# Kernel optimization log

Measured on AMD Instinct MI355X. Metric: run time of the kernel, lower is better.

The kernel has to match this reference:

```python
import jax, jax.numpy as jnp
import numpy as np

T, B, I, H, NCLS = 1024, 256, 128, 128, 18

def setup_inputs() -> dict:
    key = jax.random.key(0)
    ks = jax.random.split(key, 8)
    s = 1.0 / np.sqrt(H)  # torch nn.LSTM/Linear init bound
    inp = jax.random.normal(ks[0], (T, B, I), dtype=jnp.float32)
    hidden = jnp.zeros((1, B, H), dtype=jnp.float32)
    cell = jnp.zeros((1, B, H), dtype=jnp.float32)
    W_ih = jax.random.uniform(ks[1], (4 * H, I), jnp.float32, -s, s)
    W_hh = jax.random.uniform(ks[2], (4 * H, H), jnp.float32, -s, s)
    b_ih = jax.random.uniform(ks[3], (4 * H,), jnp.float32, -s, s)
    b_hh = jax.random.uniform(ks[4], (4 * H,), jnp.float32, -s, s)
    fc_W = jax.random.uniform(ks[5], (NCLS, H), jnp.float32, -s, s)
    fc_b = jax.random.uniform(ks[6], (NCLS,), jnp.float32, -s, s)
    return {"input": inp, "hidden": hidden, "cell": cell, "W_ih": W_ih,
            "W_hh": W_hh, "b_ih": b_ih, "b_hh": b_hh, "fc_W": fc_W, "fc_b": fc_b}

def reference(input, hidden, cell, W_ih, W_hh, b_ih, b_hh, fc_W, fc_b):
    # Single-layer unidirectional LSTM (PyTorch gate order i,f,g,o) + Linear head.
    h0, c0 = hidden[0], cell[0]  # [B,H]
    b = b_ih + b_hh

    def step(carry, x_t):
        h, c = carry
        gates = x_t @ W_ih.T + h @ W_hh.T + b  # [B,4H]
        i, f, g, o = jnp.split(gates, 4, axis=-1)
        i = jax.nn.sigmoid(i)
        f = jax.nn.sigmoid(f)
        g = jnp.tanh(g)
        o = jax.nn.sigmoid(o)
        c = f * c + i * g
        h = o * jnp.tanh(c)
        return (h, c), h

    (hT, cT), hs = jax.lax.scan(step, (h0, c0), input)  # hs: [T,B,H]
    out = hs @ fc_W.T + fc_b  # [T,B,18]
    return (out, (hT[None], cT[None]))
```

## Files before the change

kernel.cpp:

```cpp
#include <hip/hip_runtime.h>
#include <cstdint>
#include <cstddef>

#define TSTEPS 1024
#define NB 256
#define NI 128
#define NH 128
#define NC 18
#define CH 32
#define NCHUNK (TSTEPS/CH)
#define XGS 516

typedef _Float16 f16x8 __attribute__((ext_vector_type(8)));
typedef float    f32x4 __attribute__((ext_vector_type(4)));
typedef _Float16 half2_t __attribute__((ext_vector_type(2)));

__device__ __forceinline__ half2_t as_h2(uint32_t v){
  union { uint32_t u; half2_t h; } cv; cv.u = v; return cv.h;
}
__device__ __forceinline__ uint32_t pku(float a, float b){
  union { half2_t h; uint32_t u; } cv; cv.h.x=(_Float16)a; cv.h.y=(_Float16)b; return cv.u;
}
__device__ __forceinline__ float dot2f(half2_t a, half2_t b, float c){
#if __has_builtin(__builtin_amdgcn_fdot2)
  return __builtin_amdgcn_fdot2(a, b, c, false);
#else
  return c + (float)a.x*(float)b.x + (float)a.y*(float)b.y;
#endif
}
__device__ __forceinline__ float fast_rcp(float x){
#if __has_builtin(__builtin_amdgcn_rcpf)
  return __builtin_amdgcn_rcpf(x);
#else
  return 1.f / x;
#endif
}
__device__ __forceinline__ float sigm(float v){
  return fast_rcp(1.f + __expf(-v));
}
__device__ __forceinline__ float tanhx(float v){
  float r = fast_rcp(1.f + __expf(2.f*v));
  return __builtin_fmaf(-2.f, r, 1.f);
}
__device__ __forceinline__ f16x8 ldrow_f16(const float* base){
  float4 f0 = ((const float4*)base)[0];
  float4 f1 = ((const float4*)base)[1];
  f16x8 r;
  r[0]=(_Float16)f0.x; r[1]=(_Float16)f0.y; r[2]=(_Float16)f0.z; r[3]=(_Float16)f0.w;
  r[4]=(_Float16)f1.x; r[5]=(_Float16)f1.y; r[6]=(_Float16)f1.z; r[7]=(_Float16)f1.w;
  return r;
}
__device__ __forceinline__ void barrier_lds(){
  asm volatile("s_waitcnt lgkmcnt(0)" ::: "memory");
  __builtin_amdgcn_s_barrier();
}

__global__ __launch_bounds__(512, 2) void lstm_mfma(
    const float* __restrict__ x,
    const float* __restrict__ h0,
    const float* __restrict__ c0,
    const float* __restrict__ Wih,
    const float* __restrict__ Whh,
    const float* __restrict__ bih,
    const float* __restrict__ bhh,
    const float* __restrict__ fcW,
    const float* __restrict__ fcb,
    float* __restrict__ out,
    float* __restrict__ hT,
    float* __restrict__ cT)
{
  const int b    = blockIdx.x;
  const int tid  = threadIdx.x;
  const int w    = tid >> 6;
  const int l    = tid & 63;
  const int n    = l & 15;
  const int quad = l >> 4;

  __shared__ __align__(16) _Float16 xs[CH][136];
  __shared__ __align__(16) float    xgp[CH][XGS];
  __shared__ __align__(16) _Float16 hist[CH][128];
  __shared__ __align__(16) uint32_t fcw[NC][66];

  f16x8 whh[4][4], wih[4][4];
#pragma unroll
  for (int q = 0; q < 4; ++q){
    const int row = q*128 + w*16 + n;
#pragma unroll
    for (int kt = 0; kt < 4; ++kt){
      whh[q][kt] = ldrow_f16(Whh + (size_t)row*NH + kt*32 + quad*8);
      wih[q][kt] = ldrow_f16(Wih + (size_t)row*NI + kt*32 + quad*8);
    }
  }
  float biasq[4];
#pragma unroll
  for (int q = 0; q < 4; ++q){
    const int g = q*128 + w*16 + n;
    biasq[q] = bih[g] + bhh[g];
  }
  float cst = c0[(size_t)b*NH + w*16 + n];

  if (tid < 128) hist[CH-1][tid] = (_Float16)h0[(size_t)b*NH + tid];
#pragma unroll
  for (int r = 0; r < 3; ++r){
    int idx = tid + 512*r;
    if (idx < NC*64){
      int j = idx >> 6, k = idx & 63;
      float2 f = ((const float2*)(fcW + (size_t)j*NH))[k];
      fcw[j][k] = pku(f.x, f.y);
    }
  }

  const int ttA = tid >> 5;
  const int ttB = ttA + 16;
  const int k4  = tid & 31;
  float4 xpA = ((const float4*)(x + ((size_t)ttA*NB + b)*NI))[k4];
  float4 xpB = ((const float4*)(x + ((size_t)ttB*NB + b)*NI))[k4];
  __syncthreads();

  f16x8 afr[4] = { (f16x8)(_Float16)0, (f16x8)(_Float16)0,
                   (f16x8)(_Float16)0, (f16x8)(_Float16)0 };
  float hlast = 0.f;

#pragma unroll 1
  for (int ck = 0; ck < NCHUNK; ++ck){
    const int t0 = ck*CH;

    {
      union { _Float16 h[4]; uint2 u2; } pa, pb;
      pa.h[0]=(_Float16)xpA.x; pa.h[1]=(_Float16)xpA.y;
      pa.h[2]=(_Float16)xpA.z; pa.h[3]=(_Float16)xpA.w;
      *(uint2*)&xs[ttA][4*k4] = pa.u2;
      pb.h[0]=(_Float16)xpB.x; pb.h[1]=(_Float16)xpB.y;
      pb.h[2]=(_Float16)xpB.z; pb.h[3]=(_Float16)xpB.w;
      *(uint2*)&xs[ttB][4*k4] = pb.u2;
    }
    barrier_lds();

    {
      f16x8 xa[2][4];
#pragma unroll
      for (int mt = 0; mt < 2; ++mt)
#pragma unroll
        for (int kt = 0; kt < 4; ++kt)
          xa[mt][kt] = *(const f16x8*)&xs[mt*16 + n][kt*32 + quad*8];

#pragma unroll
      for (int q = 0; q < 4; ++q){
#pragma unroll
        for (int mt = 0; mt < 2; ++mt){
          f32x4 acc = { biasq[q], biasq[q], biasq[q], biasq[q] };
#pragma unroll
          for (int kt = 0; kt < 4; ++kt)
            acc = __builtin_amdgcn_mfma_f32_16x16x32_f16(xa[mt][kt], wih[q][kt], acc, 0, 0, 0);
#pragma unroll
          for (int r = 0; r < 4; ++r)
            xgp[mt*16 + quad*4 + r][(w*16 + n)*4 + q] = acc[r];
        }
      }
    }

    if (ck + 1 < NCHUNK){
      const size_t t1 = (size_t)(t0 + CH);
      xpA = ((const float4*)(x + ((t1 + ttA)*NB + b)*NI))[k4];
      xpB = ((const float4*)(x + ((t1 + ttB)*NB + b)*NI))[k4];
    }
    barrier_lds();

#pragma unroll 4
    for (int tt = 0; tt < CH; ++tt){
      f32x4 sgv = *(const f32x4*)&xgp[tt][(w*16 + n)*4];
      const int rp = (tt + CH - 1) & (CH - 1);
      if (n == 0){
#pragma unroll
        for (int kt = 0; kt < 4; ++kt)
          afr[kt] = *(const f16x8*)&hist[rp][kt*32 + quad*8];
      }
      float gate[4];
#pragma unroll
      for (int q = 0; q < 4; ++q){
        f32x4 aA; aA[0] = sgv[q];
        aA = __builtin_amdgcn_mfma_f32_16x16x32_f16(afr[0], whh[q][0], aA, 0, 0, 0);
        aA = __builtin_amdgcn_mfma_f32_16x16x32_f16(afr[1], whh[q][1], aA, 0, 0, 0);
        f32x4 aB; aB[0] = 0.f;
        aB = __builtin_amdgcn_mfma_f32_16x16x32_f16(afr[2], whh[q][2], aB, 0, 0, 0);
        aB = __builtin_amdgcn_mfma_f32_16x16x32_f16(afr[3], whh[q][3], aB, 0, 0, 0);
        gate[q] = aA[0] + aB[0];
      }
      if (l < 16){
        float iv = sigm(gate[0]);
        float fv = sigm(gate[1]);
        float gv = tanhx(gate[2]);
        float ov = sigm(gate[3]);
        cst = __builtin_fmaf(fv, cst, iv*gv);
        float hv = ov * tanhx(cst);
        hlast = hv;
        hist[tt][w*16 + l] = (_Float16)hv;
      }
      barrier_lds();
      (void)rp;
    }

    {
      const int tt = tid >> 4;
      const int jb = tid & 15;
      const uint4* hb = (const uint4*)&hist[tt][0];
#pragma unroll
      for (int jj = 0; jj < 2; ++jj){
        const int j = jj*16 + jb;
        if (j < NC){
          const uint2* fw = (const uint2*)&fcw[j][0];
          float a0=0.f, a1=0.f, a2=0.f, a3=0.f;
#pragma unroll
          for (int q = 0; q < 4; ++q){
            uint4 v0 = hb[q], v1 = hb[4+q], v2 = hb[8+q], v3 = hb[12+q];
            uint2 f0a = fw[2*q],    f0b = fw[2*q+1];
            uint2 f1a = fw[8+2*q],  f1b = fw[8+2*q+1];
            uint2 f2a = fw[16+2*q], f2b = fw[16+2*q+1];
            uint2 f3a = fw[24+2*q], f3b = fw[24+2*q+1];
            a0 = dot2f(as_h2(f0a.x), as_h2(v0.x), a0);
            a1 = dot2f(as_h2(f1a.x), as_h2(v1.x), a1);
            a2 = dot2f(as_h2(f2a.x), as_h2(v2.x), a2);
            a3 = dot2f(as_h2(f3a.x), as_h2(v3.x), a3);
            a0 = dot2f(as_h2(f0a.y), as_h2(v0.y), a0);
            a1 = dot2f(as_h2(f1a.y), as_h2(v1.y), a1);
            a2 = dot2f(as_h2(f2a.y), as_h2(v2.y), a2);
            a3 = dot2f(as_h2(f3a.y), as_h2(v3.y), a3);
            a0 = dot2f(as_h2(f0b.x), as_h2(v0.z), a0);
            a1 = dot2f(as_h2(f1b.x), as_h2(v1.z), a1);
            a2 = dot2f(as_h2(f2b.x), as_h2(v2.z), a2);
            a3 = dot2f(as_h2(f3b.x), as_h2(v3.z), a3);
            a0 = dot2f(as_h2(f0b.y), as_h2(v0.w), a0);
            a1 = dot2f(as_h2(f1b.y), as_h2(v1.w), a1);
            a2 = dot2f(as_h2(f2b.y), as_h2(v2.w), a2);
            a3 = dot2f(as_h2(f3b.y), as_h2(v3.w), a3);
          }
          out[(size_t)(t0+tt)*NB*NC + (size_t)b*NC + j] =
              (a0+a1) + (a2+a3) + fcb[j];
        }
      }
    }
  }

  if (l < 16){
    hT[(size_t)b*NH + w*16 + l] = hlast;
    cT[(size_t)b*NH + w*16 + l] = cst;
  }
}

extern "C" void kernel_launch(void* const* d_in, const int* in_sizes, int n_in,
                              void* d_out, int out_size, void* d_ws, size_t ws_size,
                              hipStream_t stream) {
  (void)in_sizes; (void)n_in; (void)d_ws; (void)ws_size; (void)out_size;
  const float* x   = (const float*)d_in[0];
  const float* h0  = (const float*)d_in[1];
  const float* c0  = (const float*)d_in[2];
  const float* Wih = (const float*)d_in[3];
  const float* Whh = (const float*)d_in[4];
  const float* bih = (const float*)d_in[5];
  const float* bhh = (const float*)d_in[6];
  const float* fcW = (const float*)d_in[7];
  const float* fcb = (const float*)d_in[8];
  float* out = (float*)d_out;
  float* hT  = out + (size_t)TSTEPS*NB*NC;
  float* cT  = hT + (size_t)NB*NH;
  hipLaunchKernelGGL(lstm_mfma, dim3(NB), dim3(512), 0, stream,
                     x, h0, c0, Wih, Whh, bih, bhh, fcW, fcb, out, hT, cT);
}
```

Before: 822.2 us.

## Interleave next-chunk input projection and FC head into the recurrent step loop

Double-buffers the x-gate buffer and the h history. The next chunk's input projection and the previous chunk's FC head are split into slices that run during idle slots of the serial per-timestep recurrence, instead of as separate phases between chunks. The goal is to hide non-recurrent work behind the latency-bound MFMA/barrier chain and remove the per-chunk serial phases. All lanes now load the h fragments every step, in place of only n==0. This adds LDS traffic and register pressure per step, and may lengthen the critical path of each timestep.

```diff
diff --git a/kernel.cpp b/kernel.cpp
--- a/kernel.cpp
+++ b/kernel.cpp
@@ -54,6 +54,57 @@
   asm volatile("s_waitcnt lgkmcnt(0)" ::: "memory");
   __builtin_amdgcn_s_barrier();
 }
+
+#define X_SLICE(Q) do {                                                          \
+    const int mt_ = s_ & 1;                                                      \
+    f16x8 xa0 = *(const f16x8*)&xs[mt_*16+n][0*32+quad*8];                       \
+    f16x8 xa1 = *(const f16x8*)&xs[mt_*16+n][1*32+quad*8];                       \
+    f16x8 xa2 = *(const f16x8*)&xs[mt_*16+n][2*32+quad*8];                       \
+    f16x8 xa3 = *(const f16x8*)&xs[mt_*16+n][3*32+quad*8];                       \
+    f32x4 acc_ = { biasq[Q], biasq[Q], biasq[Q], biasq[Q] };                     \
+    acc_ = __builtin_amdgcn_mfma_f32_16x16x32_f16(xa0, wih[Q][0], acc_, 0,0,0);  \
+    acc_ = __builtin_amdgcn_mfma_f32_16x16x32_f16(xa1, wih[Q][1], acc_, 0,0,0);  \
+    acc_ = __builtin_amdgcn_mfma_f32_16x16x32_f16(xa2, wih[Q][2], acc_, 0,0,0);  \
+    acc_ = __builtin_amdgcn_mfma_f32_16x16x32_f16(xa3, wih[Q][3], acc_, 0,0,0);  \
+    xgn[mt_*16+quad*4+0][cellw4+(Q)] = acc_[0];                                  \
+    xgn[mt_*16+quad*4+1][cellw4+(Q)] = acc_[1];                                  \
+    xgn[mt_*16+quad*4+2][cellw4+(Q)] = acc_[2];                                  \
+    xgn[mt_*16+quad*4+3][cellw4+(Q)] = acc_[3];                                  \
+  } while(0)
+
+#define HEAD_SLICE(J, ACC, FJ) do {                                              \
+    if ((J)==0 || jb+16 < NC){                                                   \
+      const int j_ = jb + 16*(J);                                                \
+      const uint4* hb_ = (const uint4*)&hist[((ckh-1)*CH + hr) & 63][0];         \
+      const uint2* fw_ = (const uint2*)&fcw[j_][0];                              \
+      uint4 v0=hb_[qh], v1=hb_[4+qh], v2=hb_[8+qh], v3=hb_[12+qh];               \
+      uint2 f0a=fw_[2*qh],    f0b=fw_[2*qh+1];                                   \
+      uint2 f1a=fw_[8+2*qh],  f1b=fw_[8+2*qh+1];                                 \
+      uint2 f2a=fw_[16+2*qh], f2b=fw_[16+2*qh+1];                                \
+      uint2 f3a=fw_[24+2*qh], f3b=fw_[24+2*qh+1];                                \
+      ACC[0]=dot2f(as_h2(f0a.x),as_h2(v0.x),ACC[0]);                             \
+      ACC[1]=dot2f(as_h2(f1a.x),as_h2(v1.x),ACC[1]);                             \
+      ACC[2]=dot2f(as_h2(f2a.x),as_h2(v2.x),ACC[2]);                             \
+      ACC[3]=dot2f(as_h2(f3a.x),as_h2(v3.x),ACC[3]);                             \
+      ACC[0]=dot2f(as_h2(f0a.y),as_h2(v0.y),ACC[0]);                             \
+      ACC[1]=dot2f(as_h2(f1a.y),as_h2(v1.y),ACC[1]);                             \
+      ACC[2]=dot2f(as_h2(f2a.y),as_h2(v2.y),ACC[2]);                             \
+      ACC[3]=dot2f(as_h2(f3a.y),as_h2(v3.y),ACC[3]);                             \
+      ACC[0]=dot2f(as_h2(f0b.x),as_h2(v0.z),ACC[0]);                             \
+      ACC[1]=dot2f(as_h2(f1b.x),as_h2(v1.z),ACC[1]);                             \
+      ACC[2]=dot2f(as_h2(f2b.x),as_h2(v2.z),ACC[2]);                             \
+      ACC[3]=dot2f(as_h2(f3b.x),as_h2(v3.z),ACC[3]);                             \
+      ACC[0]=dot2f(as_h2(f0b.y),as_h2(v0.w),ACC[0]);                             \
+      ACC[1]=dot2f(as_h2(f1b.y),as_h2(v1.w),ACC[1]);                             \
+      ACC[2]=dot2f(as_h2(f2b.y),as_h2(v2.w),ACC[2]);                             \
+      ACC[3]=dot2f(as_h2(f3b.y),as_h2(v3.w),ACC[3]);                             \
+      if (qh == 3){                                                              \
+        out[(size_t)((ckh-1)*CH + hr)*NB*NC + (size_t)b*NC + j_] =               \
+            (ACC[0]+ACC[1]) + (ACC[2]+ACC[3]) + (FJ);                            \
+        ACC[0]=0.f; ACC[1]=0.f; ACC[2]=0.f; ACC[3]=0.f;                          \
+      }                                                                          \
+    }                                                                            \
+  } while(0)
 
 __global__ __launch_bounds__(512, 2) void lstm_mfma(
     const float* __restrict__ x,
@@ -75,12 +126,12 @@
   const int l    = tid & 63;
   const int n    = l & 15;
   const int quad = l >> 4;
+  const int cellw4 = (w*16 + n)*4;
 
   __shared__ __align__(16) _Float16 xs[CH][136];
-  __shared__ __align__(16) float    xgp[CH][XGS];
-  __shared__ __align__(16) _Float16 hist[CH][128];
+  __shared__ __align__(16) float    xgp[2][CH][XGS];
+  __shared__ __align__(16) _Float16 hist[64][128];
   __shared__ __align__(16) uint32_t fcw[NC][66];
-
   f16x8 whh[4][4], wih[4][4];
 #pragma unroll
   for (int q = 0; q < 4; ++q){
@@ -99,7 +150,7 @@
   }
   float cst = c0[(size_t)b*NH + w*16 + n];
 
-  if (tid < 128) hist[CH-1][tid] = (_Float16)h0[(size_t)b*NH + tid];
+  if (tid < 128) hist[63][tid] = (_Float16)h0[(size_t)b*NH + tid];
 #pragma unroll
   for (int r = 0; r < 3; ++r){
     int idx = tid + 512*r;
@@ -110,6 +161,12 @@
     }
   }
 
+  const int jb = tid & 15;
+  const int hr = tid >> 4;
+  const float fj0 = fcb[jb];
+  const float fj1 = (jb + 16 < NC) ? fcb[jb+16] : 0.f;
+  f32x4 accH0 = {0.f,0.f,0.f,0.f}, accH1 = {0.f,0.f,0.f,0.f};
+
   const int ttA = tid >> 5;
   const int ttB = ttA + 16;
   const int k4  = tid & 31;
@@ -117,15 +174,47 @@
   float4 xpB = ((const float4*)(x + ((size_t)ttB*NB + b)*NI))[k4];
   __syncthreads();
 
-  f16x8 afr[4] = { (f16x8)(_Float16)0, (f16x8)(_Float16)0,
-                   (f16x8)(_Float16)0, (f16x8)(_Float16)0 };
+  {
+    union { _Float16 h[4]; uint2 u2; } pa, pb;
+    pa.h[0]=(_Float16)xpA.x; pa.h[1]=(_Float16)xpA.y;
+    pa.h[2]=(_Float16)xpA.z; pa.h[3]=(_Float16)xpA.w;
+    *(uint2*)&xs[ttA][4*k4] = pa.u2;
+    pb.h[0]=(_Float16)xpB.x; pb.h[1]=(_Float16)xpB.y;
+    pb.h[2]=(_Float16)xpB.z; pb.h[3]=(_Float16)xpB.w;
+    *(uint2*)&xs[ttB][4*k4] = pb.u2;
+  }
+  barrier_lds();
+
+  {
+    f16x8 xa[2][4];
+#pragma unroll
+    for (int mt = 0; mt < 2; ++mt)
+#pragma unroll
+      for (int kt = 0; kt < 4; ++kt)
+        xa[mt][kt] = *(const f16x8*)&xs[mt*16 + n][kt*32 + quad*8];
+#pragma unroll
+    for (int q = 0; q < 4; ++q){
+#pragma unroll
+      for (int mt = 0; mt < 2; ++mt){
+        f32x4 acc = { biasq[q], biasq[q], biasq[q], biasq[q] };
+#pragma unroll
+        for (int kt = 0; kt < 4; ++kt)
+          acc = __builtin_amdgcn_mfma_f32_16x16x32_f16(xa[mt][kt], wih[q][kt], acc, 0, 0, 0);
+#pragma unroll
+        for (int r = 0; r < 4; ++r)
+          xgp[0][mt*16 + quad*4 + r][cellw4 + q] = acc[r];
+      }
+    }
+  }
+  xpA = ((const float4*)(x + ((size_t)(CH+ttA)*NB + b)*NI))[k4];
+  xpB = ((const float4*)(x + ((size_t)(CH+ttB)*NB + b)*NI))[k4];
+  barrier_lds();
+
   float hlast = 0.f;
 
 #pragma unroll 1
   for (int ck = 0; ck < NCHUNK; ++ck){
-    const int t0 = ck*CH;
-
-    {
+    if (ck + 1 < NCHUNK){
       union { _Float16 h[4]; uint2 u2; } pa, pb;
       pa.h[0]=(_Float16)xpA.x; pa.h[1]=(_Float16)xpA.y;
       pa.h[2]=(_Float16)xpA.z; pa.h[3]=(_Float16)xpA.w;
@@ -135,57 +224,53 @@
       *(uint2*)&xs[ttB][4*k4] = pb.u2;
     }
     barrier_lds();
-
-    {
-      f16x8 xa[2][4];
-#pragma unroll
-      for (int mt = 0; mt < 2; ++mt)
-#pragma unroll
-        for (int kt = 0; kt < 4; ++kt)
-          xa[mt][kt] = *(const f16x8*)&xs[mt*16 + n][kt*32 + quad*8];
-
-#pragma unroll
-      for (int q = 0; q < 4; ++q){
-#pragma unroll
-        for (int mt = 0; mt < 2; ++mt){
-          f32x4 acc = { biasq[q], biasq[q], biasq[q], biasq[q] };
-#pragma unroll
-          for (int kt = 0; kt < 4; ++kt)
-            acc = __builtin_amdgcn_mfma_f32_16x16x32_f16(xa[mt][kt], wih[q][kt], acc, 0, 0, 0);
-#pragma unroll
-          for (int r = 0; r < 4; ++r)
-            xgp[mt*16 + quad*4 + r][(w*16 + n)*4 + q] = acc[r];
-        }
-      }
-    }
-
-    if (ck + 1 < NCHUNK){
-      const size_t t1 = (size_t)(t0 + CH);
-      xpA = ((const float4*)(x + ((t1 + ttA)*NB + b)*NI))[k4];
-      xpB = ((const float4*)(x + ((t1 + ttB)*NB + b)*NI))[k4];
-    }
-    barrier_lds();
+    if (ck + 2 < NCHUNK){
+      const size_t t2 = (size_t)(ck + 2)*CH;
+      xpA = ((const float4*)(x + ((t2 + ttA)*NB + b)*NI))[k4];
+      xpB = ((const float4*)(x + ((t2 + ttB)*NB + b)*NI))[k4];
+    }
+
+    float (*xgc)[XGS] = xgp[ck & 1];
+    float (*xgn)[XGS] = xgp[(ck + 1) & 1];
+    const int tbase = ck*CH;
+    const int ckh = ck;
 
 #pragma unroll 4
     for (int tt = 0; tt < CH; ++tt){
-      f32x4 sgv = *(const f32x4*)&xgp[tt][(w*16 + n)*4];
-      const int rp = (tt + CH - 1) & (CH - 1);
-      if (n == 0){
-#pragma unroll
-        for (int kt = 0; kt < 4; ++kt)
-          afr[kt] = *(const f16x8*)&hist[rp][kt*32 + quad*8];
-      }
+      f32x4 sgv = *(const f32x4*)&xgc[tt][cellw4];
+      const _Float16* hprev = &hist[(tbase + tt + 63) & 63][0];
+      f16x8 afr0 = *(const f16x8*)&hprev[0*32 + quad*8];
+      f16x8 afr1 = *(const f16x8*)&hprev[1*32 + quad*8];
+      f16x8 afr2 = *(const f16x8*)&hprev[2*32 + quad*8];
+      f16x8 afr3 = *(const f16x8*)&hprev[3*32 + quad*8];
       float gate[4];
 #pragma unroll
       for (int q = 0; q < 4; ++q){
         f32x4 aA; aA[0] = sgv[q];
-        aA = __builtin_amdgcn_mfma_f32_16x16x32_f16(afr[0], whh[q][0], aA, 0, 0, 0);
-        aA = __builtin_amdgcn_mfma_f32_16x16x32_f16(afr[1], whh[q][1], aA, 0, 0, 0);
+        aA = __builtin_amdgcn_mfma_f32_16x16x32_f16(afr0, whh[q][0], aA, 0, 0, 0);
+        aA = __builtin_amdgcn_mfma_f32_16x16x32_f16(afr1, whh[q][1], aA, 0, 0, 0);
         f32x4 aB; aB[0] = 0.f;
-        aB = __builtin_amdgcn_mfma_f32_16x16x32_f16(afr[2], whh[q][2], aB, 0, 0, 0);
-        aB = __builtin_amdgcn_mfma_f32_16x16x32_f16(afr[3], whh[q][3], aB, 0, 0, 0);
+        aB = __builtin_amdgcn_mfma_f32_16x16x32_f16(afr2, whh[q][2], aB, 0, 0, 0);
+        aB = __builtin_amdgcn_mfma_f32_16x16x32_f16(afr3, whh[q][3], aB, 0, 0, 0);
         gate[q] = aA[0] + aB[0];
       }
+
+      if ((tt & 3) == 0 && ck + 1 < NCHUNK){
+        const int s_ = tt >> 2;
+        switch (s_ >> 1){
+          case 0: X_SLICE(0); break;
+          case 1: X_SLICE(1); break;
+          case 2: X_SLICE(2); break;
+          case 3: X_SLICE(3); break;
+        }
+      }
+      if ((tt & 3) == 2 && ck >= 1){
+        const int s_ = (tt - 2) >> 2;
+        const int qh = s_ & 3;
+        if (s_ < 4) HEAD_SLICE(0, accH0, fj0);
+        else        HEAD_SLICE(1, accH1, fj1);
+      }
+
       if (l < 16){
         float iv = sigm(gate[0]);
         float fv = sigm(gate[1]);
@@ -194,50 +279,19 @@
         cst = __builtin_fmaf(fv, cst, iv*gv);
         float hv = ov * tanhx(cst);
         hlast = hv;
-        hist[tt][w*16 + l] = (_Float16)hv;
+        hist[(tbase + tt) & 63][w*16 + l] = (_Float16)hv;
       }
       barrier_lds();
-      (void)rp;
-    }
-
-    {
-      const int tt = tid >> 4;
-      const int jb = tid & 15;
-      const uint4* hb = (const uint4*)&hist[tt][0];
-#pragma unroll
-      for (int jj = 0; jj < 2; ++jj){
-        const int j = jj*16 + jb;
-        if (j < NC){
-          const uint2* fw = (const uint2*)&fcw[j][0];
-          float a0=0.f, a1=0.f, a2=0.f, a3=0.f;
-#pragma unroll
-          for (int q = 0; q < 4; ++q){
-            uint4 v0 = hb[q], v1 = hb[4+q], v2 = hb[8+q], v3 = hb[12+q];
-            uint2 f0a = fw[2*q],    f0b = fw[2*q+1];
-            uint2 f1a = fw[8+2*q],  f1b = fw[8+2*q+1];
-            uint2 f2a = fw[16+2*q], f2b = fw[16+2*q+1];
-            uint2 f3a = fw[24+2*q], f3b = fw[24+2*q+1];
-            a0 = dot2f(as_h2(f0a.x), as_h2(v0.x), a0);
-            a1 = dot2f(as_h2(f1a.x), as_h2(v1.x), a1);
-            a2 = dot2f(as_h2(f2a.x), as_h2(v2.x), a2);
-            a3 = dot2f(as_h2(f3a.x), as_h2(v3.x), a3);
-            a0 = dot2f(as_h2(f0a.y), as_h2(v0.y), a0);
-            a1 = dot2f(as_h2(f1a.y), as_h2(v1.y), a1);
-            a2 = dot2f(as_h2(f2a.y), as_h2(v2.y), a2);
-            a3 = dot2f(as_h2(f3a.y), as_h2(v3.y), a3);
-            a0 = dot2f(as_h2(f0b.x), as_h2(v0.z), a0);
-            a1 = dot2f(as_h2(f1b.x), as_h2(v1.z), a1);
-            a2 = dot2f(as_h2(f2b.x), as_h2(v2.z), a2);
-            a3 = dot2f(as_h2(f3b.x), as_h2(v3.z), a3);
-            a0 = dot2f(as_h2(f0b.y), as_h2(v0.w), a0);
-            a1 = dot2f(as_h2(f1b.y), as_h2(v1.w), a1);
-            a2 = dot2f(as_h2(f2b.y), as_h2(v2.w), a2);
-            a3 = dot2f(as_h2(f3b.y), as_h2(v3.w), a3);
-          }
-          out[(size_t)(t0+tt)*NB*NC + (size_t)b*NC + j] =
-              (a0+a1) + (a2+a3) + fcb[j];
-        }
-      }
+    }
+  }
+
+  {
+    const int ckh = NCHUNK;
+#pragma unroll
+    for (int s_ = 0; s_ < 8; ++s_){
+      const int qh = s_ & 3;
+      if (s_ < 4) HEAD_SLICE(0, accH0, fj0);
+      else        HEAD_SLICE(1, accH1, fj1);
     }
   }
 
```

Result: slower. 852.5 us (+3.7%).

## Warp-specialize LSTM: recurrent waves overlap input GEMM and FC head

Applied to the files above, without the earlier changes.

Splits the block's 8 waves into 4 recurrent waves and 4 helper waves. Each recurrent wave now owns 32 hidden cells using W_hh fragments. The helper waves hold W_ih fragments and, inside the per-timestep barrier loop, stage the next chunk of x, compute its input projection into a double-buffered xgp, and run the FC head for the previous chunk. This removes the serial per-chunk input GEMM and head phases from the critical path. It also folds log2e scaling into the weights so the activations can use exp2, and XOR-swizzles the 64-row hidden history. The cost is that each recurrent wave does twice the MFMA work per step, and the helper work must fit inside the recurrent step time.

```diff
diff --git a/kernel.cpp b/kernel.cpp
--- a/kernel.cpp
+++ b/kernel.cpp
@@ -11,6 +11,9 @@
 #define NCHUNK (TSTEPS/CH)
 #define XGS 516
 
+#define LOG2E_F    1.44269504088896f
+#define TWO_LOG2E_F 2.88539008177793f
+
 typedef _Float16 f16x8 __attribute__((ext_vector_type(8)));
 typedef float    f32x4 __attribute__((ext_vector_type(4)));
 typedef _Float16 half2_t __attribute__((ext_vector_type(2)));
@@ -35,25 +38,72 @@
   return 1.f / x;
 #endif
 }
-__device__ __forceinline__ float sigm(float v){
-  return fast_rcp(1.f + __expf(-v));
-}
-__device__ __forceinline__ float tanhx(float v){
-  float r = fast_rcp(1.f + __expf(2.f*v));
-  return __builtin_fmaf(-2.f, r, 1.f);
-}
-__device__ __forceinline__ f16x8 ldrow_f16(const float* base){
+__device__ __forceinline__ float exp2x(float v){
+#if __has_builtin(__builtin_amdgcn_exp2f)
+  return __builtin_amdgcn_exp2f(v);
+#else
+  return __expf(v * 0.6931471805599453f);
+#endif
+}
+__device__ __forceinline__ float sigm2(float vp){
+  return fast_rcp(1.f + exp2x(-vp));
+}
+__device__ __forceinline__ float tanh2p(float vp){
+  return __builtin_fmaf(-2.f, fast_rcp(1.f + exp2x(vp)), 1.f);
+}
+__device__ __forceinline__ f16x8 ldrow_f16s(const float* base, float s){
   float4 f0 = ((const float4*)base)[0];
   float4 f1 = ((const float4*)base)[1];
   f16x8 r;
-  r[0]=(_Float16)f0.x; r[1]=(_Float16)f0.y; r[2]=(_Float16)f0.z; r[3]=(_Float16)f0.w;
-  r[4]=(_Float16)f1.x; r[5]=(_Float16)f1.y; r[6]=(_Float16)f1.z; r[7]=(_Float16)f1.w;
+  r[0]=(_Float16)(f0.x*s); r[1]=(_Float16)(f0.y*s); r[2]=(_Float16)(f0.z*s); r[3]=(_Float16)(f0.w*s);
+  r[4]=(_Float16)(f1.x*s); r[5]=(_Float16)(f1.y*s); r[6]=(_Float16)(f1.z*s); r[7]=(_Float16)(f1.w*s);
   return r;
 }
 __device__ __forceinline__ void barrier_lds(){
   asm volatile("s_waitcnt lgkmcnt(0)" ::: "memory");
   __builtin_amdgcn_s_barrier();
 }
+
+#define H_GEMM_TILE(CT, MT_, XGN) do {                                             \
+    const _Float16* xr_ = &xs[(MT_)*16 + n][0];                                    \
+    f16x8 xa0_ = *(const f16x8*)&xr_[ 0 + quad*8];                                 \
+    f16x8 xa1_ = *(const f16x8*)&xr_[32 + quad*8];                                 \
+    f16x8 xa2_ = *(const f16x8*)&xr_[64 + quad*8];                                 \
+    f16x8 xa3_ = *(const f16x8*)&xr_[96 + quad*8];                                 \
+    f32x4 acc_ = { biash[CT], biash[CT], biash[CT], biash[CT] };                   \
+    acc_ = __builtin_amdgcn_mfma_f32_16x16x32_f16(xa0_, wfr[CT][0], acc_, 0,0,0);  \
+    acc_ = __builtin_amdgcn_mfma_f32_16x16x32_f16(xa1_, wfr[CT][1], acc_, 0,0,0);  \
+    acc_ = __builtin_amdgcn_mfma_f32_16x16x32_f16(xa2_, wfr[CT][2], acc_, 0,0,0);  \
+    acc_ = __builtin_amdgcn_mfma_f32_16x16x32_f16(xa3_, wfr[CT][3], acc_, 0,0,0);  \
+    float* xw_ = &(XGN)[(MT_)*16 + quad*4][((CT)*16 + n)*4 + hq];                  \
+    xw_[0] = acc_[0]; xw_[XGS] = acc_[1]; xw_[2*XGS] = acc_[2]; xw_[3*XGS] = acc_[3]; \
+  } while(0)
+
+#define STAGE_W(M_, XPV) do {                                                      \
+    union { _Float16 h_[4]; uint2 u_; } pk_;                                       \
+    pk_.h_[0]=(_Float16)(XPV).x; pk_.h_[1]=(_Float16)(XPV).y;                      \
+    pk_.h_[2]=(_Float16)(XPV).z; pk_.h_[3]=(_Float16)(XPV).w;                      \
+    *(uint2*)&xs[hrW][4*(k8 + 8*(M_))] = pk_.u_;                                   \
+  } while(0)
+
+#define HEAD_DOT(JV, CKH, FB) do {                                                 \
+    const int row_ = (((CKH)*CH + hrW) & 63);                                      \
+    const uint4* hb_ = (const uint4*)&hist[row_][0];                               \
+    const int hx4_ = row_ & 7;                                                     \
+    const uint2* fw_ = (const uint2*)&fcw[(JV)][0];                                \
+    float a0_=0.f, a1_=0.f, a2_=0.f, a3_=0.f;                                      \
+    _Pragma("unroll")                                                              \
+    for (int k_ = 0; k_ < 16; ++k_){                                               \
+      uint4 v_ = hb_[k_ ^ hx4_];                                                   \
+      uint2 fa_ = fw_[2*k_], fb2_ = fw_[2*k_+1];                                   \
+      a0_ = dot2f(as_h2(fa_.x),  as_h2(v_.x), a0_);                                \
+      a1_ = dot2f(as_h2(fa_.y),  as_h2(v_.y), a1_);                                \
+      a2_ = dot2f(as_h2(fb2_.x), as_h2(v_.z), a2_);                                \
+      a3_ = dot2f(as_h2(fb2_.y), as_h2(v_.w), a3_);                                \
+    }                                                                              \
+    out[(size_t)((CKH)*CH + hrW)*NB*NC + (size_t)b*NC + (JV)] =                    \
+        (a0_+a1_) + (a2_+a3_) + (FB);                                              \
+  } while(0)
 
 __global__ __launch_bounds__(512, 2) void lstm_mfma(
     const float* __restrict__ x,
@@ -75,31 +125,52 @@
   const int l    = tid & 63;
   const int n    = l & 15;
   const int quad = l >> 4;
+  const bool isR = (w < 4);
+  const bool hi  = (l >= 32);
 
   __shared__ __align__(16) _Float16 xs[CH][136];
-  __shared__ __align__(16) float    xgp[CH][XGS];
-  __shared__ __align__(16) _Float16 hist[CH][128];
+  __shared__ __align__(16) float    xgp[2][CH][XGS];
+  __shared__ __align__(16) _Float16 hist[64][128];
   __shared__ __align__(16) uint32_t fcw[NC][66];
 
-  f16x8 whh[4][4], wih[4][4];
-#pragma unroll
-  for (int q = 0; q < 4; ++q){
-    const int row = q*128 + w*16 + n;
-#pragma unroll
-    for (int kt = 0; kt < 4; ++kt){
-      whh[q][kt] = ldrow_f16(Whh + (size_t)row*NH + kt*32 + quad*8);
-      wih[q][kt] = ldrow_f16(Wih + (size_t)row*NI + kt*32 + quad*8);
+  const int hq   = w - 4;
+  const int tid2 = hq*64 + l;
+  const int hrW  = tid2 >> 3;
+  const int k8   = tid2 & 7;
+  const int jb   = k8;
+
+  float4 xp0, xp1, xp2, xp3;
+  if (!isR){
+    const float* xb = x + ((size_t)hrW*NB + b)*NI;
+    xp0 = ((const float4*)xb)[k8];
+    xp1 = ((const float4*)xb)[k8+8];
+    xp2 = ((const float4*)xb)[k8+16];
+    xp3 = ((const float4*)xb)[k8+24];
+  }
+
+  f16x8 wfr[8][4];
+  float biash[8];
+  {
+    const float* wsrc = isR ? Whh : Wih;
+#pragma unroll
+    for (int f = 0; f < 8; ++f){
+      const int g  = isR ? ((f>>1)*128 + w*32 + (f&1)*16 + n)
+                         : (hq*128 + f*16 + n);
+      const int qq = isR ? (f>>1) : hq;
+      const float sc = (qq == 2) ? TWO_LOG2E_F : LOG2E_F;
+#pragma unroll
+      for (int kt = 0; kt < 4; ++kt)
+        wfr[f][kt] = ldrow_f16s(wsrc + (size_t)g*128 + kt*32 + quad*8, sc);
+      biash[f] = (bih[g] + bhh[g]) * sc;
     }
   }
-  float biasq[4];
-#pragma unroll
-  for (int q = 0; q < 4; ++q){
-    const int g = q*128 + w*16 + n;
-    biasq[q] = bih[g] + bhh[g];
-  }
-  float cst = c0[(size_t)b*NH + w*16 + n];
-
-  if (tid < 128) hist[CH-1][tid] = (_Float16)h0[(size_t)b*NH + tid];
+
+  const int mycell = (isR ? w*32 : 0) + (hi ? 16 : 0) + n;
+  float cst = 0.f;
+  if (isR) cst = c0[(size_t)b*NH + mycell];
+  float hlast = 0.f;
+
+  if (tid < 128) hist[63][tid ^ 56] = (_Float16)h0[(size_t)b*NH + tid];
 #pragma unroll
   for (int r = 0; r < 3; ++r){
     int idx = tid + 512*r;
@@ -109,141 +180,132 @@
       fcw[j][k] = pku(f.x, f.y);
     }
   }
-
-  const int ttA = tid >> 5;
-  const int ttB = ttA + 16;
-  const int k4  = tid & 31;
-  float4 xpA = ((const float4*)(x + ((size_t)ttA*NB + b)*NI))[k4];
-  float4 xpB = ((const float4*)(x + ((size_t)ttB*NB + b)*NI))[k4];
-  __syncthreads();
-
-  f16x8 afr[4] = { (f16x8)(_Float16)0, (f16x8)(_Float16)0,
-                   (f16x8)(_Float16)0, (f16x8)(_Float16)0 };
-  float hlast = 0.f;
+  float fj0 = 0.f, fj1 = 0.f, fj2 = 0.f;
+  if (!isR){ fj0 = fcb[jb]; fj1 = fcb[jb+8]; if (jb < 2) fj2 = fcb[16+jb]; }
+
+  if (!isR){ STAGE_W(0, xp0); STAGE_W(1, xp1); STAGE_W(2, xp2); STAGE_W(3, xp3); }
+  barrier_lds();
+
+  if (!isR){
+    float (*xgn)[XGS] = xgp[0];
+#pragma unroll
+    for (int ct = 0; ct < 8; ++ct)
+#pragma unroll
+      for (int mt = 0; mt < 2; ++mt)
+        H_GEMM_TILE(ct, mt, xgn);
+    const float* xb = x + ((size_t)(CH + hrW)*NB + b)*NI;
+    xp0 = ((const float4*)xb)[k8];
+    xp1 = ((const float4*)xb)[k8+8];
+    xp2 = ((const float4*)xb)[k8+16];
+    xp3 = ((const float4*)xb)[k8+24];
+  }
+  barrier_lds();
 
 #pragma unroll 1
   for (int ck = 0; ck < NCHUNK; ++ck){
-    const int t0 = ck*CH;
-
-    {
-      union { _Float16 h[4]; uint2 u2; } pa, pb;
-      pa.h[0]=(_Float16)xpA.x; pa.h[1]=(_Float16)xpA.y;
-      pa.h[2]=(_Float16)xpA.z; pa.h[3]=(_Float16)xpA.w;
-      *(uint2*)&xs[ttA][4*k4] = pa.u2;
-      pb.h[0]=(_Float16)xpB.x; pb.h[1]=(_Float16)xpB.y;
-      pb.h[2]=(_Float16)xpB.z; pb.h[3]=(_Float16)xpB.w;
-      *(uint2*)&xs[ttB][4*k4] = pb.u2;
-    }
-    barrier_lds();
-
-    {
-      f16x8 xa[2][4];
-#pragma unroll
-      for (int mt = 0; mt < 2; ++mt)
-#pragma unroll
-        for (int kt = 0; kt < 4; ++kt)
-          xa[mt][kt] = *(const f16x8*)&xs[mt*16 + n][kt*32 + quad*8];
-
-#pragma unroll
-      for (int q = 0; q < 4; ++q){
-#pragma unroll
-        for (int mt = 0; mt < 2; ++mt){
-          f32x4 acc = { biasq[q], biasq[q], biasq[q], biasq[q] };
-#pragma unroll
-          for (int kt = 0; kt < 4; ++kt)
-            acc = __builtin_amdgcn_mfma_f32_16x16x32_f16(xa[mt][kt], wih[q][kt], acc, 0, 0, 0);
-#pragma unroll
-          for (int r = 0; r < 4; ++r)
-            xgp[mt*16 + quad*4 + r][(w*16 + n)*4 + q] = acc[r];
+    float (*xgc)[XGS] = xgp[ck & 1];
+    float (*xgn)[XGS] = xgp[(ck + 1) & 1];
+    const int tbase = (ck*CH) & 63;
+
+#pragma unroll 4
+    for (int tt = 0; tt < CH; ++tt){
+      if (isR){
+        const int rrow = (tbase + tt + 63) & 63;
+        const int hx = (rrow & 7) << 3;
+        const _Float16* hp = &hist[rrow][0];
+        f16x8 a0 = *(const f16x8*)&hp[( 0 + quad*8) ^ hx];
+        f16x8 a1 = *(const f16x8*)&hp[(32 + quad*8) ^ hx];
+        f16x8 a2 = *(const f16x8*)&hp[(64 + quad*8) ^ hx];
+        f16x8 a3 = *(const f16x8*)&hp[(96 + quad*8) ^ hx];
+        const int cb4 = (w*32 + n)*4;
+        f32x4 sgA = *(const f32x4*)&xgc[tt][cb4];
+        f32x4 sgB = *(const f32x4*)&xgc[tt][cb4 + 64];
+        float gA[4], gB[4];
+        __builtin_amdgcn_s_setprio(1);
+#pragma unroll
+        for (int q = 0; q < 4; ++q){
+          f32x4 aA; aA[0] = sgA[q];
+          aA = __builtin_amdgcn_mfma_f32_16x16x32_f16(a0, wfr[q*2+0][0], aA, 0,0,0);
+          aA = __builtin_amdgcn_mfma_f32_16x16x32_f16(a1, wfr[q*2+0][1], aA, 0,0,0);
+          f32x4 aB; aB[0] = 0.f;
+          aB = __builtin_amdgcn_mfma_f32_16x16x32_f16(a2, wfr[q*2+0][2], aB, 0,0,0);
+          aB = __builtin_amdgcn_mfma_f32_16x16x32_f16(a3, wfr[q*2+0][3], aB, 0,0,0);
+          gA[q] = aA[0] + aB[0];
+        }
+#pragma unroll
+        for (int q = 0; q < 4; ++q){
+          f32x4 aA; aA[0] = sgB[q];
+          aA = __builtin_amdgcn_mfma_f32_16x16x32_f16(a0, wfr[q*2+1][0], aA, 0,0,0);
+          aA = __builtin_amdgcn_mfma_f32_16x16x32_f16(a1, wfr[q*2+1][1], aA, 0,0,0);
+          f32x4 aB; aB[0] = 0.f;
+          aB = __builtin_amdgcn_mfma_f32_16x16x32_f16(a2, wfr[q*2+1][2], aB, 0,0,0);
+          aB = __builtin_amdgcn_mfma_f32_16x16x32_f16(a3, wfr[q*2+1][3], aB, 0,0,0);
+          gB[q] = aA[0] + aB[0];
+        }
+        __builtin_amdgcn_s_setprio(0);
+        float gi = hi ? gB[0] : gA[0];
+        float gf = hi ? gB[1] : gA[1];
+        float gg = hi ? gB[2] : gA[2];
+        float go = hi ? gB[3] : gA[3];
+        float iv = sigm2(gi);
+        float fv = sigm2(gf);
+        float gv = tanh2p(gg);
+        float ov = sigm2(go);
+        cst = __builtin_fmaf(fv, cst, iv*gv);
+        float hv = ov * tanh2p(cst * TWO_LOG2E_F);
+        hlast = hv;
+        const int wrow = (tbase + tt) & 63;
+        if ((l & 31) < 16)
+          hist[wrow][mycell ^ ((wrow & 7) << 3)] = (_Float16)hv;
+      } else {
+        if (tt == 0){
+          if (ck <= NCHUNK-2){ STAGE_W(0, xp0); STAGE_W(1, xp1); }
+        } else if (tt == 1){
+          if (ck <= NCHUNK-2){ STAGE_W(2, xp2); STAGE_W(3, xp3); }
+        } else if (tt == 3){
+          if (ck <= NCHUNK-3){
+            const float* xb = x + ((size_t)((ck+2)*CH + hrW)*NB + b)*NI;
+            xp0 = ((const float4*)xb)[k8];
+            xp1 = ((const float4*)xb)[k8+8];
+            xp2 = ((const float4*)xb)[k8+16];
+            xp3 = ((const float4*)xb)[k8+24];
+          }
+        } else if (tt >= 4 && tt < 20){
+          if (ck <= NCHUNK-2){
+            const int slice_ = tt - 4;
+            const int mt_ = slice_ & 1;
+            switch (slice_ >> 1){
+              case 0: H_GEMM_TILE(0, mt_, xgn); break;
+              case 1: H_GEMM_TILE(1, mt_, xgn); break;
+              case 2: H_GEMM_TILE(2, mt_, xgn); break;
+              case 3: H_GEMM_TILE(3, mt_, xgn); break;
+              case 4: H_GEMM_TILE(4, mt_, xgn); break;
+              case 5: H_GEMM_TILE(5, mt_, xgn); break;
+              case 6: H_GEMM_TILE(6, mt_, xgn); break;
+              case 7: H_GEMM_TILE(7, mt_, xgn); break;
+            }
+          }
+        } else if (tt == 20){
+          if (ck >= 1) HEAD_DOT(jb, ck-1, fj0);
+        } else if (tt == 21){
+          if (ck >= 1) HEAD_DOT(jb+8, ck-1, fj1);
+        } else if (tt == 22){
+          if (ck >= 1 && jb < 2) HEAD_DOT(16+jb, ck-1, fj2);
         }
       }
+      barrier_lds();
     }
-
-    if (ck + 1 < NCHUNK){
-      const size_t t1 = (size_t)(t0 + CH);
-      xpA = ((const float4*)(x + ((t1 + ttA)*NB + b)*NI))[k4];
-      xpB = ((const float4*)(x + ((t1 + ttB)*NB + b)*NI))[k4];
+  }
+
+  if (isR){
+    if ((l & 31) < 16){
+      hT[(size_t)b*NH + mycell] = hlast;
+      cT[(size_t)b*NH + mycell] = cst;
     }
-    barrier_lds();
-
-#pragma unroll 4
-    for (int tt = 0; tt < CH; ++tt){
-      f32x4 sgv = *(const f32x4*)&xgp[tt][(w*16 + n)*4];
-      const int rp = (tt + CH - 1) & (CH - 1);
-      if (n == 0){
-#pragma unroll
-        for (int kt = 0; kt < 4; ++kt)
-          afr[kt] = *(const f16x8*)&hist[rp][kt*32 + quad*8];
-      }
-      float gate[4];
-#pragma unroll
-      for (int q = 0; q < 4; ++q){
-        f32x4 aA; aA[0] = sgv[q];
-        aA = __builtin_amdgcn_mfma_f32_16x16x32_f16(afr[0], whh[q][0], aA, 0, 0, 0);
-        aA = __builtin_amdgcn_mfma_f32_16x16x32_f16(afr[1], whh[q][1], aA, 0, 0, 0);
-        f32x4 aB; aB[0] = 0.f;
-        aB = __builtin_amdgcn_mfma_f32_16x16x32_f16(afr[2], whh[q][2], aB, 0, 0, 0);
-        aB = __builtin_amdgcn_mfma_f32_16x16x32_f16(afr[3], whh[q][3], aB, 0, 0, 0);
-        gate[q] = aA[0] + aB[0];
-      }
-      if (l < 16){
-        float iv = sigm(gate[0]);
-        float fv = sigm(gate[1]);
-        float gv = tanhx(gate[2]);
-        float ov = sigm(gate[3]);
-        cst = __builtin_fmaf(fv, cst, iv*gv);
-        float hv = ov * tanhx(cst);
-        hlast = hv;
-        hist[tt][w*16 + l] = (_Float16)hv;
-      }
-      barrier_lds();
-      (void)rp;
-    }
-
-    {
-      const int tt = tid >> 4;
-      const int jb = tid & 15;
-      const uint4* hb = (const uint4*)&hist[tt][0];
-#pragma unroll
-      for (int jj = 0; jj < 2; ++jj){
-        const int j = jj*16 + jb;
-        if (j < NC){
-          const uint2* fw = (const uint2*)&fcw[j][0];
-          float a0=0.f, a1=0.f, a2=0.f, a3=0.f;
-#pragma unroll
-          for (int q = 0; q < 4; ++q){
-            uint4 v0 = hb[q], v1 = hb[4+q], v2 = hb[8+q], v3 = hb[12+q];
-            uint2 f0a = fw[2*q],    f0b = fw[2*q+1];
-            uint2 f1a = fw[8+2*q],  f1b = fw[8+2*q+1];
-            uint2 f2a = fw[16+2*q], f2b = fw[16+2*q+1];
-            uint2 f3a = fw[24+2*q], f3b = fw[24+2*q+1];
-            a0 = dot2f(as_h2(f0a.x), as_h2(v0.x), a0);
-            a1 = dot2f(as_h2(f1a.x), as_h2(v1.x), a1);
-            a2 = dot2f(as_h2(f2a.x), as_h2(v2.x), a2);
-            a3 = dot2f(as_h2(f3a.x), as_h2(v3.x), a3);
-            a0 = dot2f(as_h2(f0a.y), as_h2(v0.y), a0);
-            a1 = dot2f(as_h2(f1a.y), as_h2(v1.y), a1);
-            a2 = dot2f(as_h2(f2a.y), as_h2(v2.y), a2);
-            a3 = dot2f(as_h2(f3a.y), as_h2(v3.y), a3);
-            a0 = dot2f(as_h2(f0b.x), as_h2(v0.z), a0);
-            a1 = dot2f(as_h2(f1b.x), as_h2(v1.z), a1);
-            a2 = dot2f(as_h2(f2b.x), as_h2(v2.z), a2);
-            a3 = dot2f(as_h2(f3b.x), as_h2(v3.z), a3);
-            a0 = dot2f(as_h2(f0b.y), as_h2(v0.w), a0);
-            a1 = dot2f(as_h2(f1b.y), as_h2(v1.w), a1);
-            a2 = dot2f(as_h2(f2b.y), as_h2(v2.w), a2);
-            a3 = dot2f(as_h2(f3b.y), as_h2(v3.w), a3);
-          }
-          out[(size_t)(t0+tt)*NB*NC + (size_t)b*NC + j] =
-              (a0+a1) + (a2+a3) + fcb[j];
-        }
-      }
-    }
-  }
-
-  if (l < 16){
-    hT[(size_t)b*NH + w*16 + l] = hlast;
-    cT[(size_t)b*NH + w*16 + l] = cst;
+  } else {
+    HEAD_DOT(jb, NCHUNK-1, fj0);
+    HEAD_DOT(jb+8, NCHUNK-1, fj1);
+    if (jb < 2) HEAD_DOT(16+jb, NCHUNK-1, fj2);
   }
 }
 
```

Measured after the change: 879.0 us. 1.07x slower.

## Interleave gate rows so all lanes compute activations via DPP quad broadcast

Applied to the files above, without the earlier changes.

Gate rows are remapped so each group of four adjacent lanes holds the i, f, g and o pre-activations for one hidden cell. That spreads the nonlinearity work across all 64 lanes instead of 16 lanes doing four activations serially. The log2(e) scale factors are folded into the weights and bias, so each activation needs only a single exp2 and reciprocal with a lane-dependent sign and affine fixup. Gate values are then exchanged with DPP quad broadcasts. The per-step h fragment load is now done by every lane unconditionally, and fp16 rounding of the pre-scaled weights slightly changes precision.

```diff
diff --git a/kernel.cpp b/kernel.cpp
--- a/kernel.cpp
+++ b/kernel.cpp
@@ -11,6 +11,9 @@
 #define NCHUNK (TSTEPS/CH)
 #define XGS 516
 
+#define LOG2E_F     1.44269504088896f
+#define TWO_LOG2E_F 2.88539008177793f
+
 typedef _Float16 f16x8 __attribute__((ext_vector_type(8)));
 typedef float    f32x4 __attribute__((ext_vector_type(4)));
 typedef _Float16 half2_t __attribute__((ext_vector_type(2)));
@@ -35,19 +38,29 @@
   return 1.f / x;
 #endif
 }
-__device__ __forceinline__ float sigm(float v){
-  return fast_rcp(1.f + __expf(-v));
-}
-__device__ __forceinline__ float tanhx(float v){
-  float r = fast_rcp(1.f + __expf(2.f*v));
-  return __builtin_fmaf(-2.f, r, 1.f);
-}
-__device__ __forceinline__ f16x8 ldrow_f16(const float* base){
+__device__ __forceinline__ float exp2x(float v){
+#if __has_builtin(__builtin_amdgcn_exp2f)
+  return __builtin_amdgcn_exp2f(v);
+#else
+  return __expf(v * 0.6931471805599453f);
+#endif
+}
+template<int CTRL>
+__device__ __forceinline__ float qbcast(float v){
+#if __has_builtin(__builtin_amdgcn_mov_dpp)
+  union { float f; int i; } u; u.f = v;
+  u.i = __builtin_amdgcn_mov_dpp(u.i, CTRL, 0xF, 0xF, false);
+  return u.f;
+#else
+  return __shfl(v, ((threadIdx.x & 63) & ~3) + (CTRL & 3), 64);
+#endif
+}
+__device__ __forceinline__ f16x8 ldrow_f16s(const float* base, float s){
   float4 f0 = ((const float4*)base)[0];
   float4 f1 = ((const float4*)base)[1];
   f16x8 r;
-  r[0]=(_Float16)f0.x; r[1]=(_Float16)f0.y; r[2]=(_Float16)f0.z; r[3]=(_Float16)f0.w;
-  r[4]=(_Float16)f1.x; r[5]=(_Float16)f1.y; r[6]=(_Float16)f1.z; r[7]=(_Float16)f1.w;
+  r[0]=(_Float16)(f0.x*s); r[1]=(_Float16)(f0.y*s); r[2]=(_Float16)(f0.z*s); r[3]=(_Float16)(f0.w*s);
+  r[4]=(_Float16)(f1.x*s); r[5]=(_Float16)(f1.y*s); r[6]=(_Float16)(f1.z*s); r[7]=(_Float16)(f1.w*s);
   return r;
 }
 __device__ __forceinline__ void barrier_lds(){
@@ -75,29 +88,35 @@
   const int l    = tid & 63;
   const int n    = l & 15;
   const int quad = l >> 4;
+  const int q4   = l & 3;
+  const int c4   = (l >> 2) & 3;
 
   __shared__ __align__(16) _Float16 xs[CH][136];
   __shared__ __align__(16) float    xgp[CH][XGS];
   __shared__ __align__(16) _Float16 hist[CH][128];
   __shared__ __align__(16) uint32_t fcw[NC][66];
 
+  const float sc = (q4 == 2) ? TWO_LOG2E_F : LOG2E_F;
   f16x8 whh[4][4], wih[4][4];
-#pragma unroll
-  for (int q = 0; q < 4; ++q){
-    const int row = q*128 + w*16 + n;
+  float biasv[4];
+#pragma unroll
+  for (int m = 0; m < 4; ++m){
+    const int row = q4*128 + w*16 + 4*m + c4;
 #pragma unroll
     for (int kt = 0; kt < 4; ++kt){
-      whh[q][kt] = ldrow_f16(Whh + (size_t)row*NH + kt*32 + quad*8);
-      wih[q][kt] = ldrow_f16(Wih + (size_t)row*NI + kt*32 + quad*8);
-    }
+      whh[m][kt] = ldrow_f16s(Whh + (size_t)row*NH + kt*32 + quad*8, sc);
+      wih[m][kt] = ldrow_f16s(Wih + (size_t)row*NI + kt*32 + quad*8, sc);
+    }
+    biasv[m] = (bih[row] + bhh[row]) * sc;
   }
-  float biasq[4];
-#pragma unroll
-  for (int q = 0; q < 4; ++q){
-    const int g = q*128 + w*16 + n;
-    biasq[q] = bih[g] + bhh[g];
-  }
-  float cst = c0[(size_t)b*NH + w*16 + n];
+
+  const uint32_t smask = (q4 == 2) ? 0u : 0x80000000u;
+  const float aK = (q4 == 2) ? 1.f : 0.f;
+  const float sK = (q4 == 2) ? -2.f : 1.f;
+
+  const int mycell = w*16 + quad*4 + c4;
+  float cst = c0[(size_t)b*NH + mycell];
+  float hlast = 0.f;
 
   if (tid < 128) hist[CH-1][tid] = (_Float16)h0[(size_t)b*NH + tid];
 #pragma unroll
@@ -116,10 +135,6 @@
   float4 xpA = ((const float4*)(x + ((size_t)ttA*NB + b)*NI))[k4];
   float4 xpB = ((const float4*)(x + ((size_t)ttB*NB + b)*NI))[k4];
   __syncthreads();
-
-  f16x8 afr[4] = { (f16x8)(_Float16)0, (f16x8)(_Float16)0,
-                   (f16x8)(_Float16)0, (f16x8)(_Float16)0 };
-  float hlast = 0.f;
 
 #pragma unroll 1
   for (int ck = 0; ck < NCHUNK; ++ck){
@@ -145,16 +160,16 @@
           xa[mt][kt] = *(const f16x8*)&xs[mt*16 + n][kt*32 + quad*8];
 
 #pragma unroll
-      for (int q = 0; q < 4; ++q){
+      for (int m = 0; m < 4; ++m){
 #pragma unroll
         for (int mt = 0; mt < 2; ++mt){
-          f32x4 acc = { biasq[q], biasq[q], biasq[q], biasq[q] };
+          f32x4 acc = { biasv[m], biasv[m], biasv[m], biasv[m] };
 #pragma unroll
           for (int kt = 0; kt < 4; ++kt)
-            acc = __builtin_amdgcn_mfma_f32_16x16x32_f16(xa[mt][kt], wih[q][kt], acc, 0, 0, 0);
+            acc = __builtin_amdgcn_mfma_f32_16x16x32_f16(xa[mt][kt], wih[m][kt], acc, 0, 0, 0);
 #pragma unroll
           for (int r = 0; r < 4; ++r)
-            xgp[mt*16 + quad*4 + r][(w*16 + n)*4 + q] = acc[r];
+            xgp[mt*16 + quad*4 + r][w*64 + n*4 + m] = acc[r];
         }
       }
     }
@@ -168,36 +183,73 @@
 
 #pragma unroll 4
     for (int tt = 0; tt < CH; ++tt){
-      f32x4 sgv = *(const f32x4*)&xgp[tt][(w*16 + n)*4];
+      f32x4 sgv = *(const f32x4*)&xgp[tt][w*64 + n*4];
       const int rp = (tt + CH - 1) & (CH - 1);
-      if (n == 0){
-#pragma unroll
-        for (int kt = 0; kt < 4; ++kt)
-          afr[kt] = *(const f16x8*)&hist[rp][kt*32 + quad*8];
-      }
-      float gate[4];
-#pragma unroll
-      for (int q = 0; q < 4; ++q){
-        f32x4 aA; aA[0] = sgv[q];
-        aA = __builtin_amdgcn_mfma_f32_16x16x32_f16(afr[0], whh[q][0], aA, 0, 0, 0);
-        aA = __builtin_amdgcn_mfma_f32_16x16x32_f16(afr[1], whh[q][1], aA, 0, 0, 0);
-        f32x4 aB; aB[0] = 0.f;
-        aB = __builtin_amdgcn_mfma_f32_16x16x32_f16(afr[2], whh[q][2], aB, 0, 0, 0);
-        aB = __builtin_amdgcn_mfma_f32_16x16x32_f16(afr[3], whh[q][3], aB, 0, 0, 0);
-        gate[q] = aA[0] + aB[0];
-      }
-      if (l < 16){
-        float iv = sigm(gate[0]);
-        float fv = sigm(gate[1]);
-        float gv = tanhx(gate[2]);
-        float ov = sigm(gate[3]);
-        cst = __builtin_fmaf(fv, cst, iv*gv);
-        float hv = ov * tanhx(cst);
-        hlast = hv;
-        hist[tt][w*16 + l] = (_Float16)hv;
-      }
+      const _Float16* hprev = &hist[rp][0];
+      f16x8 a0 = *(const f16x8*)&hprev[ 0 + quad*8];
+      f16x8 a1 = *(const f16x8*)&hprev[32 + quad*8];
+      f16x8 a2 = *(const f16x8*)&hprev[64 + quad*8];
+      f16x8 a3 = *(const f16x8*)&hprev[96 + quad*8];
+      float g0, g1, g2, g3;
+      {
+        f32x4 aA, aB;
+        aA[0] = sgv[0];
+        aA = __builtin_amdgcn_mfma_f32_16x16x32_f16(a0, whh[0][0], aA, 0, 0, 0);
+        aA = __builtin_amdgcn_mfma_f32_16x16x32_f16(a1, whh[0][1], aA, 0, 0, 0);
+        aB[0] = 0.f;
+        aB = __builtin_amdgcn_mfma_f32_16x16x32_f16(a2, whh[0][2], aB, 0, 0, 0);
+        aB = __builtin_amdgcn_mfma_f32_16x16x32_f16(a3, whh[0][3], aB, 0, 0, 0);
+        g0 = aA[0] + aB[0];
+      }
+      {
+        f32x4 aA, aB;
+        aA[0] = sgv[1];
+        aA = __builtin_amdgcn_mfma_f32_16x16x32_f16(a0, whh[1][0], aA, 0, 0, 0);
+        aA = __builtin_amdgcn_mfma_f32_16x16x32_f16(a1, whh[1][1], aA, 0, 0, 0);
+        aB[0] = 0.f;
+        aB = __builtin_amdgcn_mfma_f32_16x16x32_f16(a2, whh[1][2], aB, 0, 0, 0);
+        aB = __builtin_amdgcn_mfma_f32_16x16x32_f16(a3, whh[1][3], aB, 0, 0, 0);
+        g1 = aA[0] + aB[0];
+      }
+      {
+        f32x4 aA, aB;
+        aA[0] = sgv[2];
+        aA = __builtin_amdgcn_mfma_f32_16x16x32_f16(a0, whh[2][0], aA, 0, 0, 0);
+        aA = __builtin_amdgcn_mfma_f32_16x16x32_f16(a1, whh[2][1], aA, 0, 0, 0);
+        aB[0] = 0.f;
+        aB = __builtin_amdgcn_mfma_f32_16x16x32_f16(a2, whh[2][2], aB, 0, 0, 0);
+        aB = __builtin_amdgcn_mfma_f32_16x16x32_f16(a3, whh[2][3], aB, 0, 0, 0);
+        g2 = aA[0] + aB[0];
+      }
+      {
+        f32x4 aA, aB;
+        aA[0] = sgv[3];
+        aA = __builtin_amdgcn_mfma_f32_16x16x32_f16(a0, whh[3][0], aA, 0, 0, 0);
+        aA = __builtin_amdgcn_mfma_f32_16x16x32_f16(a1, whh[3][1], aA, 0, 0, 0);
+        aB[0] = 0.f;
+        aB = __builtin_amdgcn_mfma_f32_16x16x32_f16(a2, whh[3][2], aB, 0, 0, 0);
+        aB = __builtin_amdgcn_mfma_f32_16x16x32_f16(a3, whh[3][3], aB, 0, 0, 0);
+        g3 = aA[0] + aB[0];
+      }
+      const bool qlo = (quad & 1) != 0;
+      const bool qhi = (quad & 2) != 0;
+      float gsel = qhi ? (qlo ? g3 : g2) : (qlo ? g1 : g0);
+      union { float f; uint32_t u; } gx; gx.f = gsel; gx.u ^= smask;
+      float ev  = exp2x(gx.f);
+      float rr  = fast_rcp(1.f + ev);
+      float act = __builtin_fmaf(sK, rr, aK);
+      float vi = qbcast<0x00>(act);
+      float vf = qbcast<0x55>(act);
+      float vg = qbcast<0xAA>(act);
+      float vo = qbcast<0xFF>(act);
+      cst = __builtin_fmaf(vf, cst, vi*vg);
+      float e2 = exp2x(cst * TWO_LOG2E_F);
+      float tc = __builtin_fmaf(-2.f, fast_rcp(1.f + e2), 1.f);
+      float hv = vo * tc;
+      hlast = hv;
+      if (q4 == 0)
+        hist[tt][mycell] = (_Float16)hv;
       barrier_lds();
-      (void)rp;
     }
 
     {
@@ -241,9 +293,9 @@
     }
   }
 
-  if (l < 16){
-    hT[(size_t)b*NH + w*16 + l] = hlast;
-    cT[(size_t)b*NH + w*16 + l] = cst;
+  if (q4 == 0){
+    hT[(size_t)b*NH + mycell] = hlast;
+    cT[(size_t)b*NH + mycell] = cst;
   }
 }
 
```

New measurement: 723.4 us. 1.14x faster.
